# Performance work log

Measured on AMD Instinct MI355X. Metric: run time of the kernel, lower is better.

## Reference

```python
import jax, jax.numpy as jnp
import numpy as np

T, D, E, K = 8192, 4096, 64, 8


def setup_inputs() -> dict:
    key = jax.random.key(0)
    k1, k2, k3, k4 = jax.random.split(key, 4)
    x = jax.random.normal(k1, (T, D), dtype=jnp.float32)
    # nn.Linear stores weight as [out_features, in_features]
    Wg = jax.random.normal(k2, (E, D), dtype=jnp.float32) * (1.0 / np.sqrt(D))
    Wc = jax.random.normal(k3, (E, D), dtype=jnp.float32) * (1.0 / np.sqrt(D))
    extra_scale = jnp.zeros((E,), dtype=jnp.float32)  # init zeros as in module
    extra_bias = jax.random.normal(k4, (E,), dtype=jnp.float32) * 0.01
    return {"x": x, "Wg": Wg, "Wc": Wc, "extra_scale": extra_scale,
            "extra_bias": extra_bias, "topk": K}


def reference(x, Wg, Wc, extra_scale, extra_bias, topk):
    # scores = |classifier(x) * silu(gate(x))|, softmax in fp32
    gate = jnp.einsum('td,ed->te', x, Wg)        # [T, E]
    cls = jnp.einsum('td,ed->te', x, Wc)         # [T, E]
    scores = jnp.abs(cls * jax.nn.silu(gate))
    scores = jax.nn.softmax(scores.astype(jnp.float32), axis=-1)
    biased = scores + extra_bias[None, :]        # load-balance bias, used only for selection
    _, indices = jax.lax.top_k(biased, topk)     # [T, K]
    original = 1.0 + scores * extra_scale[None, :]
    weights = jnp.take_along_axis(original, indices, axis=1)  # [T, K]
    return weights.astype(x.dtype), indices
```

## Files before the change

### kernel.cpp

```cpp
#include <hip/hip_runtime.h>
#include <math.h>


#define T_DIM 8192
#define D_DIM 4096
#define E_DIM 64
#define N2    128
#define KTOP  8
#define MB_ROWS 64

#define LDS_H2S 512
#define LDS_PS  1040
#define LDS_RGS (3 * LDS_PS)
#define LDS_BFS (2 * LDS_RGS)

typedef __attribute__((ext_vector_type(8)))  short bfrag8;
typedef __attribute__((ext_vector_type(16))) float f32x16;
typedef __attribute__((ext_vector_type(4)))  float f4;

__device__ __forceinline__ unsigned short f2bf_rne(float f) {
    unsigned int u = __float_as_uint(f);
    unsigned int r = u + 0x7fffu + ((u >> 16) & 1u);
    return (unsigned short)(r >> 16);
}
__device__ __forceinline__ float bf2f(unsigned short h) {
    return __uint_as_float(((unsigned int)h) << 16);
}
__device__ __forceinline__ void split3(float v, unsigned short& h,
                                       unsigned short& m, unsigned short& l) {
    h = f2bf_rne(v);
    const float r1 = v - bf2f(h);
    m = f2bf_rne(r1);
    const float r2 = r1 - bf2f(m);
    l = f2bf_rne(r2);
}

__global__ __launch_bounds__(256)
void router_prep(const float* __restrict__ Wg, const float* __restrict__ Wc,
                 unsigned short* __restrict__ Wpk)
{
    const int t   = blockIdx.x * 256 + threadIdx.x;
    const int col = t >> 9;
    const int ch  = t & 511;
    const int k   = ch << 3;

    const float* src = (col < E_DIM) ? (Wg + (size_t)col * D_DIM)
                                     : (Wc + (size_t)(col - E_DIM) * D_DIM);
    const float4 w0 = ((const float4*)(src + k))[0];
    const float4 w1 = ((const float4*)(src + k))[1];
    const float v[8] = {w0.x, w0.y, w0.z, w0.w, w1.x, w1.y, w1.z, w1.w};

    unsigned short hv[8], mv[8], lv[8];
    #pragma unroll
    for (int j = 0; j < 8; ++j) split3(v[j], hv[j], mv[j], lv[j]);

    const int k32 = k >> 5, h2 = (k >> 4) & 1, lh = (k >> 3) & 1;
    const int n = col >> 5, lane = lh * 32 + (col & 31);
    const size_t base = ((((size_t)k32 * 4 + n) * 3 + 0) * 2 + h2) * 512 + (size_t)lane * 8;
    *(ushort4*)(Wpk + base)          = make_ushort4(hv[0], hv[1], hv[2], hv[3]);
    *(ushort4*)(Wpk + base + 4)      = make_ushort4(hv[4], hv[5], hv[6], hv[7]);
    *(ushort4*)(Wpk + base + 1024)   = make_ushort4(mv[0], mv[1], mv[2], mv[3]);
    *(ushort4*)(Wpk + base + 1028)   = make_ushort4(mv[4], mv[5], mv[6], mv[7]);
    *(ushort4*)(Wpk + base + 2048)   = make_ushort4(lv[0], lv[1], lv[2], lv[3]);
    *(ushort4*)(Wpk + base + 2052)   = make_ushort4(lv[4], lv[5], lv[6], lv[7]);
}

__global__ __launch_bounds__(512, 8)
void router_gemm(const float* __restrict__ x,
                 const unsigned short* __restrict__ Wpk,
                 float* __restrict__ P,
                 int sliceK)
{
    __shared__ unsigned short sF[2 * LDS_BFS];

    const int tid  = threadIdx.x;
    const int lane = tid & 63;
    const int wid  = tid >> 6;
    const int rg   = wid >> 2;
    const int wc   = wid & 3;
    const int l31  = lane & 31;
    const int lh   = lane >> 5;
    const int mb   = blockIdx.x;
    const int ks   = blockIdx.y;
    const int k0   = ks * sliceK;
    const int NT   = sliceK >> 5;
    const int brow0 = mb * MB_ROWS;

    const int srow = tid >> 3;
    const int kq   = tid & 7;
    const int rgs  = srow >> 5;
    const int h2w  = kq >> 2;
    const int lew  = ((kq >> 1) & 1) * 32 + (srow & 31);
    const int jw   = (kq & 1) * 4;
    const int wbase = rgs * LDS_RGS + h2w * LDS_H2S + lew * 8 + jw;
    const float* gsrc = x + (size_t)(brow0 + srow) * D_DIM + k0 + kq * 4;

    f32x16 acc;
    #pragma unroll
    for (int r = 0; r < 16; ++r) acc[r] = 0.f;

    #define WRITE_ONE(v_, bf_)                                                   \
        {                                                                        \
            ushort4 hv_, mv_, lv_;                                               \
            unsigned short h_, m_, l_;                                           \
            split3((v_).x, h_, m_, l_); hv_.x = h_; mv_.x = m_; lv_.x = l_;      \
            split3((v_).y, h_, m_, l_); hv_.y = h_; mv_.y = m_; lv_.y = l_;      \
            split3((v_).z, h_, m_, l_); hv_.z = h_; mv_.z = m_; lv_.z = l_;      \
            split3((v_).w, h_, m_, l_); hv_.w = h_; mv_.w = m_; lv_.w = l_;      \
            const int o_ = (bf_) * LDS_BFS + wbase;                              \
            *(ushort4*)&sF[o_]              = hv_;                               \
            *(ushort4*)&sF[o_ + LDS_PS]     = mv_;                               \
            *(ushort4*)&sF[o_ + 2 * LDS_PS] = lv_;                               \
        }

    {
        const f4 v0 = __builtin_nontemporal_load((const f4*)gsrc);
        WRITE_ONE(v0, 0);
    }
    asm volatile("s_waitcnt lgkmcnt(0)" ::: "memory");
    __builtin_amdgcn_s_barrier();

    for (int t = 0; t < NT; ++t) {
        const int bf = t & 1;
        const int fbase = bf * LDS_BFS + rg * LDS_RGS;
        const size_t k32 = (size_t)((k0 + t * 32) >> 5);
        const bool more = (t + 1 < NT);

        const unsigned short* bb0 =
            Wpk + ((((k32 * 4 + wc) * 3 + 0) * 2 + 0) * 64 + lane) * 8;
        const bfrag8 bh0 = *(const bfrag8*)(bb0);
        const bfrag8 bm0 = *(const bfrag8*)(bb0 + 1024);
        const bfrag8 bl0 = *(const bfrag8*)(bb0 + 2048);
        const unsigned short* bb1 = bb0 + 512;
        const bfrag8 BH1 = *(const bfrag8*)(bb1);
        const bfrag8 BM1 = *(const bfrag8*)(bb1 + 1024);
        const bfrag8 BL1 = *(const bfrag8*)(bb1 + 2048);

        f4 xa;
        if (more) xa = __builtin_nontemporal_load((const f4*)(gsrc + (t + 1) * 32));

        {
            const int ab0 = fbase + 0 * LDS_H2S + lane * 8;
            const bfrag8 ah = *(const bfrag8*)&sF[ab0];
            const bfrag8 am = *(const bfrag8*)&sF[ab0 + LDS_PS];
            const bfrag8 al = *(const bfrag8*)&sF[ab0 + 2 * LDS_PS];
            acc = __builtin_amdgcn_mfma_f32_32x32x16_bf16(ah, bl0, acc, 0, 0, 0);
            acc = __builtin_amdgcn_mfma_f32_32x32x16_bf16(al, bh0, acc, 0, 0, 0);
            acc = __builtin_amdgcn_mfma_f32_32x32x16_bf16(am, bm0, acc, 0, 0, 0);
            acc = __builtin_amdgcn_mfma_f32_32x32x16_bf16(ah, bm0, acc, 0, 0, 0);
            acc = __builtin_amdgcn_mfma_f32_32x32x16_bf16(am, bh0, acc, 0, 0, 0);
            acc = __builtin_amdgcn_mfma_f32_32x32x16_bf16(ah, bh0, acc, 0, 0, 0);
        }
        {
            const int ab1 = fbase + 1 * LDS_H2S + lane * 8;
            const bfrag8 ah = *(const bfrag8*)&sF[ab1];
            const bfrag8 am = *(const bfrag8*)&sF[ab1 + LDS_PS];
            const bfrag8 al = *(const bfrag8*)&sF[ab1 + 2 * LDS_PS];
            acc = __builtin_amdgcn_mfma_f32_32x32x16_bf16(ah, BL1, acc, 0, 0, 0);
            acc = __builtin_amdgcn_mfma_f32_32x32x16_bf16(al, BH1, acc, 0, 0, 0);
            acc = __builtin_amdgcn_mfma_f32_32x32x16_bf16(am, BM1, acc, 0, 0, 0);
            acc = __builtin_amdgcn_mfma_f32_32x32x16_bf16(ah, BM1, acc, 0, 0, 0);
            acc = __builtin_amdgcn_mfma_f32_32x32x16_bf16(am, BH1, acc, 0, 0, 0);
            acc = __builtin_amdgcn_mfma_f32_32x32x16_bf16(ah, BH1, acc, 0, 0, 0);
        }

        if (more) WRITE_ONE(xa, bf ^ 1);
        asm volatile("s_waitcnt lgkmcnt(0)" ::: "memory");
        __builtin_amdgcn_s_barrier();
    }
    #undef WRITE_ONE

    float* Pb = P + ((size_t)ks * T_DIM + brow0 + rg * 32) * N2 + wc * 32 + l31;
    #pragma unroll
    for (int r = 0; r < 16; ++r) {
        const int wrow = (r & 3) + 8 * (r >> 2) + 4 * lh;
        __builtin_nontemporal_store(acc[r], &Pb[(size_t)wrow * N2]);
    }
}

__global__ __launch_bounds__(256)
void router_topk(const float* __restrict__ P,
                 const float* __restrict__ scale,
                 const float* __restrict__ bias,
                 float* __restrict__ out,
                 int ksplit)
{
    const int lane = threadIdx.x & 63;
    const int wid  = threadIdx.x >> 6;
    const int row  = blockIdx.x * 4 + wid;

    float g = 0.f, c = 0.f;
    for (int ks = 0; ks < ksplit; ++ks) {
        const float* p = P + ((size_t)ks * T_DIM + row) * N2;
        g += p[lane];
        c += p[E_DIM + lane];
    }
    const float sg = g / (1.f + expf(-g));
    const float v  = fabsf(c * sg);

    float m = v;
    #pragma unroll
    for (int off = 32; off >= 1; off >>= 1) m = fmaxf(m, __shfl_xor(m, off));
    const float e = expf(v - m);
    float Z = e;
    #pragma unroll
    for (int off = 32; off >= 1; off >>= 1) Z += __shfl_xor(Z, off);
    const float s = e / Z;

    const float sc  = scale[lane];
    float cur = s + bias[lane];

    float myw = 0.f; int myi = 0;
    #pragma unroll
    for (int j = 0; j < KTOP; ++j) {
        float bv = cur; int bi = lane;
        #pragma unroll
        for (int off = 32; off >= 1; off >>= 1) {
            const float ov = __shfl_xor(bv, off);
            const int   oi = __shfl_xor(bi, off);
            if (ov > bv || (ov == bv && oi < bi)) { bv = ov; bi = oi; }
        }
        const float s_bi  = __shfl(s,  bi);
        const float sc_bi = __shfl(sc, bi);
        const float w = 1.f + s_bi * sc_bi;
        if (lane == j)  { myw = w; myi = bi; }
        if (lane == bi) cur = -INFINITY;
    }

    if (lane < KTOP) {
        out[(size_t)row * KTOP + lane] = myw;
        out[(size_t)T_DIM * KTOP + (size_t)row * KTOP + lane] = (float)myi;
    }
}

extern "C" void kernel_launch(void* const* d_in, const int* in_sizes, int n_in,
                              void* d_out, int out_size, void* d_ws, size_t ws_size,
                              hipStream_t stream)
{
    const float* x  = (const float*)d_in[0];
    const float* Wg = (const float*)d_in[1];
    const float* Wc = (const float*)d_in[2];
    const float* sc = (const float*)d_in[3];
    const float* bs = (const float*)d_in[4];
    float* out = (float*)d_out;
    float* P   = (float*)d_ws;

    const size_t PER = (size_t)T_DIM * N2 * sizeof(float);
    const size_t WSP = (size_t)N2 * D_DIM * sizeof(unsigned short);

    int S = 8;
    while (S > 1 && (size_t)S * PER + 3 * WSP > ws_size) S >>= 1;
    const int sliceK = D_DIM / S;

    unsigned short* Wpk = (unsigned short*)((char*)d_ws + (size_t)S * PER);

    router_prep<<<256, 256, 0, stream>>>(Wg, Wc, Wpk);
    router_gemm<<<dim3(T_DIM / MB_ROWS, S), 512, 0, stream>>>(x, Wpk, P, sliceK);
    router_topk<<<T_DIM / 4, 256, 0, stream>>>(P, sc, bs, out, S);
}
```

Before: 254.8 us.

## Software-pipeline B fragment and x loads one step ahead with double registers

Measured after the change: 261.4 us. +2.6%, slower.

```diff
diff --git a/kernel.cpp b/kernel.cpp
--- a/kernel.cpp
+++ b/kernel.cpp
@@ -65,7 +65,7 @@
     *(ushort4*)(Wpk + base + 2052)   = make_ushort4(lv[4], lv[5], lv[6], lv[7]);
 }
 
-__global__ __launch_bounds__(512, 8)
+__global__ __launch_bounds__(512, 4)
 void router_gemm(const float* __restrict__ x,
                  const unsigned short* __restrict__ Wpk,
                  float* __restrict__ P,
@@ -113,62 +113,92 @@
             *(ushort4*)&sF[o_ + 2 * LDS_PS] = lv_;                               \
         }
 
+    #define LOAD_B(P_, k32_)                                                     \
+        {                                                                        \
+            const unsigned short* bb0_ =                                         \
+                Wpk + (((((size_t)(k32_)) * 4 + wc) * 3) * 2 * 64 + (size_t)lane) * 8; \
+            P_##h0 = *(const bfrag8*)(bb0_);                                     \
+            P_##m0 = *(const bfrag8*)(bb0_ + 1024);                              \
+            P_##l0 = *(const bfrag8*)(bb0_ + 2048);                              \
+            P_##h1 = *(const bfrag8*)(bb0_ + 512);                               \
+            P_##m1 = *(const bfrag8*)(bb0_ + 1536);                              \
+            P_##l1 = *(const bfrag8*)(bb0_ + 2560);                              \
+        }
+
+    #define MFMA_STEP(bf_, P_)                                                   \
+        {                                                                        \
+            const int fb_ = (bf_) * LDS_BFS + rg * LDS_RGS;                      \
+            __builtin_amdgcn_s_setprio(1);                                       \
+            {                                                                    \
+                const int ab = fb_ + lane * 8;                                   \
+                const bfrag8 ah = *(const bfrag8*)&sF[ab];                       \
+                const bfrag8 am = *(const bfrag8*)&sF[ab + LDS_PS];              \
+                const bfrag8 al = *(const bfrag8*)&sF[ab + 2 * LDS_PS];          \
+                acc = __builtin_amdgcn_mfma_f32_32x32x16_bf16(ah, P_##l0, acc, 0, 0, 0); \
+                acc = __builtin_amdgcn_mfma_f32_32x32x16_bf16(al, P_##h0, acc, 0, 0, 0); \
+                acc = __builtin_amdgcn_mfma_f32_32x32x16_bf16(am, P_##m0, acc, 0, 0, 0); \
+                acc = __builtin_amdgcn_mfma_f32_32x32x16_bf16(ah, P_##m0, acc, 0, 0, 0); \
+                acc = __builtin_amdgcn_mfma_f32_32x32x16_bf16(am, P_##h0, acc, 0, 0, 0); \
+                acc = __builtin_amdgcn_mfma_f32_32x32x16_bf16(ah, P_##h0, acc, 0, 0, 0); \
+            }                                                                    \
+            {                                                                    \
+                const int ab = fb_ + LDS_H2S + lane * 8;                         \
+                const bfrag8 ah = *(const bfrag8*)&sF[ab];                       \
+                const bfrag8 am = *(const bfrag8*)&sF[ab + LDS_PS];              \
+                const bfrag8 al = *(const bfrag8*)&sF[ab + 2 * LDS_PS];          \
+                acc = __builtin_amdgcn_mfma_f32_32x32x16_bf16(ah, P_##l1, acc, 0, 0, 0); \
+                acc = __builtin_amdgcn_mfma_f32_32x32x16_bf16(al, P_##h1, acc, 0, 0, 0); \
+                acc = __builtin_amdgcn_mfma_f32_32x32x16_bf16(am, P_##m1, acc, 0, 0, 0); \
+                acc = __builtin_amdgcn_mfma_f32_32x32x16_bf16(ah, P_##m1, acc, 0, 0, 0); \
+                acc = __builtin_amdgcn_mfma_f32_32x32x16_bf16(am, P_##h1, acc, 0, 0, 0); \
+                acc = __builtin_amdgcn_mfma_f32_32x32x16_bf16(ah, P_##h1, acc, 0, 0, 0); \
+            }                                                                    \
+            __builtin_amdgcn_s_setprio(0);                                       \
+        }
+
+    bfrag8 Ah0, Am0, Al0, Ah1, Am1, Al1;
+    bfrag8 Bh0, Bm0, Bl0, Bh1, Bm1, Bl1;
+
     {
         const f4 v0 = __builtin_nontemporal_load((const f4*)gsrc);
         WRITE_ONE(v0, 0);
     }
+    LOAD_B(A, (k0 >> 5));
+    const int t1c = (1 < NT) ? 1 : 0;
+    f4 xa = __builtin_nontemporal_load((const f4*)(gsrc + t1c * 32));
+    f4 xb;
     asm volatile("s_waitcnt lgkmcnt(0)" ::: "memory");
     __builtin_amdgcn_s_barrier();
 
-    for (int t = 0; t < NT; ++t) {
-        const int bf = t & 1;
-        const int fbase = bf * LDS_BFS + rg * LDS_RGS;
-        const size_t k32 = (size_t)((k0 + t * 32) >> 5);
-        const bool more = (t + 1 < NT);
-
-        const unsigned short* bb0 =
-            Wpk + ((((k32 * 4 + wc) * 3 + 0) * 2 + 0) * 64 + lane) * 8;
-        const bfrag8 bh0 = *(const bfrag8*)(bb0);
-        const bfrag8 bm0 = *(const bfrag8*)(bb0 + 1024);
-        const bfrag8 bl0 = *(const bfrag8*)(bb0 + 2048);
-        const unsigned short* bb1 = bb0 + 512;
-        const bfrag8 BH1 = *(const bfrag8*)(bb1);
-        const bfrag8 BM1 = *(const bfrag8*)(bb1 + 1024);
-        const bfrag8 BL1 = *(const bfrag8*)(bb1 + 2048);
-
-        f4 xa;
-        if (more) xa = __builtin_nontemporal_load((const f4*)(gsrc + (t + 1) * 32));
-
+    for (int t = 0; t < NT; t += 2) {
         {
-            const int ab0 = fbase + 0 * LDS_H2S + lane * 8;
-            const bfrag8 ah = *(const bfrag8*)&sF[ab0];
-            const bfrag8 am = *(const bfrag8*)&sF[ab0 + LDS_PS];
-            const bfrag8 al = *(const bfrag8*)&sF[ab0 + 2 * LDS_PS];
-            acc = __builtin_amdgcn_mfma_f32_32x32x16_bf16(ah, bl0, acc, 0, 0, 0);
-            acc = __builtin_amdgcn_mfma_f32_32x32x16_bf16(al, bh0, acc, 0, 0, 0);
-            acc = __builtin_amdgcn_mfma_f32_32x32x16_bf16(am, bm0, acc, 0, 0, 0);
-            acc = __builtin_amdgcn_mfma_f32_32x32x16_bf16(ah, bm0, acc, 0, 0, 0);
-            acc = __builtin_amdgcn_mfma_f32_32x32x16_bf16(am, bh0, acc, 0, 0, 0);
-            acc = __builtin_amdgcn_mfma_f32_32x32x16_bf16(ah, bh0, acc, 0, 0, 0);
+            const int tb = (t + 1 < NT) ? t + 1 : t;
+            LOAD_B(B, ((k0 + tb * 32) >> 5));
+            const int tx = (t + 2 < NT) ? t + 2 : NT - 1;
+            xb = __builtin_nontemporal_load((const f4*)(gsrc + tx * 32));
+
+            MFMA_STEP(0, A);
+
+            if (t + 1 < NT) WRITE_ONE(xa, 1);
+            asm volatile("s_waitcnt lgkmcnt(0)" ::: "memory");
+            __builtin_amdgcn_s_barrier();
         }
         {
-            const int ab1 = fbase + 1 * LDS_H2S + lane * 8;
-            const bfrag8 ah = *(const bfrag8*)&sF[ab1];
-            const bfrag8 am = *(const bfrag8*)&sF[ab1 + LDS_PS];
-            const bfrag8 al = *(const bfrag8*)&sF[ab1 + 2 * LDS_PS];
-            acc = __builtin_amdgcn_mfma_f32_32x32x16_bf16(ah, BL1, acc, 0, 0, 0);
-            acc = __builtin_amdgcn_mfma_f32_32x32x16_bf16(al, BH1, acc, 0, 0, 0);
-            acc = __builtin_amdgcn_mfma_f32_32x32x16_bf16(am, BM1, acc, 0, 0, 0);
-            acc = __builtin_amdgcn_mfma_f32_32x32x16_bf16(ah, BM1, acc, 0, 0, 0);
-            acc = __builtin_amdgcn_mfma_f32_32x32x16_bf16(am, BH1, acc, 0, 0, 0);
-            acc = __builtin_amdgcn_mfma_f32_32x32x16_bf16(ah, BH1, acc, 0, 0, 0);
-        }
-
-        if (more) WRITE_ONE(xa, bf ^ 1);
-        asm volatile("s_waitcnt lgkmcnt(0)" ::: "memory");
-        __builtin_amdgcn_s_barrier();
+            const int tb = (t + 2 < NT) ? t + 2 : t + 1;
+            LOAD_B(A, ((k0 + tb * 32) >> 5));
+            const int tx = (t + 3 < NT) ? t + 3 : NT - 1;
+            xa = __builtin_nontemporal_load((const f4*)(gsrc + tx * 32));
+
+            MFMA_STEP(1, B);
+
+            if (t + 2 < NT) WRITE_ONE(xb, 0);
+            asm volatile("s_waitcnt lgkmcnt(0)" ::: "memory");
+            __builtin_amdgcn_s_barrier();
+        }
     }
     #undef WRITE_ONE
+    #undef LOAD_B
+    #undef MFMA_STEP
 
     float* Pb = P + ((size_t)ks * T_DIM + brow0 + rg * 32) * N2 + wc * 32 + l31;
     #pragma unroll
```
